# Kernel optimization log

Measured on AMD Instinct MI355X. Metric: run time of the kernel, lower is better.

Reference implementation:

```python
import jax, jax.numpy as jnp
import numpy as np

K = 5            # carafe kernel size
CK = 3           # content conv kernel size = max(3, K-2)
EMB = 64         # embedding size
FILTERS = 128    # output filters


def conv1x1(x, w, b=None):
    y = jnp.einsum('bhwc,co->bhwo', x, w)
    return y if b is None else y + b


def conv_same(x, w, b):
    y = jax.lax.conv_general_dilated(x, w, (1, 1), 'SAME',
                                     dimension_numbers=('NHWC', 'HWIO', 'NHWC'))
    return y + b


def up2(x):
    return jnp.repeat(jnp.repeat(x, 2, axis=1), 2, axis=2)


def setup_inputs() -> dict:
    key = jax.random.key(0)
    ks = jax.random.split(key, 12)
    B, H, W, Cf = 2, 128, 128, 128
    h, w, Cc = 64, 64, 128
    s = 0.05
    return {
        'fine': jax.random.normal(ks[0], (B, H, W, Cf), jnp.float32),
        'coarse': jax.random.normal(ks[1], (B, h, w, Cc), jnp.float32),
        # gate 1x1 conv (Cc -> 1)
        'w_gate': jax.random.normal(ks[2], (Cc, 1), jnp.float32) * s,
        'b_gate': jnp.zeros((1,), jnp.float32),
        # SemiShift: fine 1x1 (no bias), coarse 1x1 (bias), shared content conv (EMB -> K*K)
        'w_sfine': jax.random.normal(ks[3], (Cf, EMB), jnp.float32) * s,
        'w_scoarse': jax.random.normal(ks[4], (Cc, EMB), jnp.float32) * s,
        'b_scoarse': jnp.zeros((EMB,), jnp.float32),
        'w_content': jax.random.normal(ks[5], (CK, CK, EMB, K * K), jnp.float32) * s,
        'b_content': jnp.zeros((K * K,), jnp.float32),
        # output 1x1 convs
        'w_coarse': jax.random.normal(ks[6], (Cc, FILTERS), jnp.float32) * s,
        'b_coarse': jnp.zeros((FILTERS,), jnp.float32),
        'w_fineout': jax.random.normal(ks[7], (FILTERS, FILTERS), jnp.float32) * s,
        'b_fineout': jnp.zeros((FILTERS,), jnp.float32),
    }


def reference(fine, coarse, w_gate, b_gate, w_sfine, w_scoarse, b_scoarse,
              w_content, b_content, w_coarse, b_coarse, w_fineout, b_fineout):
    B, h, w, Cc = coarse.shape
    H, W = fine.shape[1], fine.shape[2]

    # gate branch
    gate = jax.nn.sigmoid(conv1x1(coarse, w_gate, b_gate))
    gate = up2(gate)  # [B,H,W,1]

    # SemiShift kernel prediction
    f = conv1x1(fine, w_sfine)                     # no bias
    f = conv_same(f, w_content, b_content)         # [B,H,W,K*K]
    c = conv1x1(coarse, w_scoarse, b_scoarse)
    c = conv_same(c, w_content, b_content)         # [B,h,w,K*K]
    kernel = jax.nn.softmax(f + up2(c), axis=-1)   # [B,H,W,K*K]

    # CarafeConvolution: extract_patches (TF layout: [pos, ch] innermost) + NN up + grouped matmul
    p = K // 2
    xp = jnp.pad(coarse, ((0, 0), (p, p), (p, p), (0, 0)))
    patches = jnp.stack([xp[:, r:r + h, cc:cc + w, :]
                         for r in range(K) for cc in range(K)], axis=3)  # [B,h,w,K*K,Cc]
    patches = patches.reshape(B, h, w, K * K * Cc)
    patches = up2(patches)                          # [B,H,W,K*K*Cc]
    # faithful reshape as in source (group_size=1): (B,H,W,Cc,K*K)
    feat = patches.reshape(B, H, W, Cc, K * K)
    carafe = jnp.einsum('bhwck,bhwk->bhwc', feat, kernel)  # [B,H,W,Cc]

    coarse_out = conv1x1(carafe, w_coarse, b_coarse)        # [B,H,W,FILTERS]
    fine_out = conv1x1(coarse_out, w_fineout, b_fineout)    # note: applied to coarse_out as in source
    return gate * fine_out + (1.0 - gate) * coarse_out
```

## Files before the change

kernel.cpp:

```cpp
#include <hip/hip_runtime.h>
#include <hip/hip_bf16.h>
#include <cstdint>
#include <cstddef>

#define KSZ 5
#define KK 25
#define EMB 64
#define CC 128
#define FILTERS 128

typedef __attribute__((ext_vector_type(8))) short short8;
typedef __attribute__((ext_vector_type(4))) float floatx4;

__device__ inline unsigned short f32_to_bf16(float f) {
    union { float f; unsigned u; } v; v.f = f;
    unsigned u = v.u;
    unsigned r = u + 0x7FFF + ((u >> 16) & 1);
    return (unsigned short)(r >> 16);
}

#define XS_P 136
__global__ __launch_bounds__(256) void embed_both_kernel(
        const float* __restrict__ xf, const float* __restrict__ wsf,
        const float* __restrict__ xc, const float* __restrict__ wsc,
        const float* __restrict__ bias_c,
        unsigned short* __restrict__ yf, unsigned short* __restrict__ yc,
        int nf, int nemb,
        const float* __restrict__ w_content, const float* __restrict__ w_coarse,
        const float* __restrict__ w_fineout,
        unsigned short* __restrict__ wconT, unsigned short* __restrict__ wcT,
        unsigned short* __restrict__ wfT) {
    int tid = threadIdx.x;

    if ((int)blockIdx.x >= nemb) {
        int idx = (blockIdx.x - nemb) * 256 + tid;
        if (idx < 18432) {
            int n = idx / 576, k = idx - n * 576;
            float v = (n < 25) ? w_content[k * 25 + n] : 0.0f;
            wconT[idx] = f32_to_bf16(v);
        } else if (idx < 34816) {
            int j = idx - 18432;
            int o = j >> 7, k = j & 127;
            wcT[j] = f32_to_bf16(w_coarse[k * 128 + o]);
        } else {
            int j = idx - 34816;
            int o = j >> 7, k = j & 127;
            wfT[j] = f32_to_bf16(w_fineout[k * 128 + o]);
        }
        return;
    }

    __shared__ unsigned short Xs[128 * XS_P];
    __shared__ unsigned short Ws[64 * XS_P];
    bool is_f = (int)blockIdx.x < nf;
    int blk = is_f ? blockIdx.x : (blockIdx.x - nf);
    const float* x = is_f ? xf : xc;
    const float* wsrcf = is_f ? wsf : wsc;
    const float* bias = is_f ? nullptr : bias_c;
    unsigned short* y = is_f ? yf : yc;
    size_t row0 = (size_t)blk * 128;

    {
        const float4* src = (const float4*)(x + row0 * 128);
        for (int ci = tid; ci < 4096; ci += 256) {
            int r = ci >> 5, c4 = ci & 31;
            float4 v = src[ci];
            uint2 u;
            u.x = (unsigned)f32_to_bf16(v.x) | ((unsigned)f32_to_bf16(v.y) << 16);
            u.y = (unsigned)f32_to_bf16(v.z) | ((unsigned)f32_to_bf16(v.w) << 16);
            *(uint2*)(&Xs[r * XS_P + c4 * 4]) = u;
        }
        for (int ci = tid; ci < 2048; ci += 256) {
            int k = ci >> 4;
            int n4 = (ci & 15) * 4;
            float4 v = *(const float4*)(wsrcf + k * 64 + n4);
            Ws[(n4 + 0) * XS_P + k] = f32_to_bf16(v.x);
            Ws[(n4 + 1) * XS_P + k] = f32_to_bf16(v.y);
            Ws[(n4 + 2) * XS_P + k] = f32_to_bf16(v.z);
            Ws[(n4 + 3) * XS_P + k] = f32_to_bf16(v.w);
        }
    }
    __syncthreads();

    int wid = tid >> 6, lane = tid & 63;
    int lr = lane & 15, hi = lane >> 4, lk = hi * 8;

    floatx4 acc[2][4];
    #pragma unroll
    for (int mi = 0; mi < 2; ++mi)
        #pragma unroll
        for (int ni = 0; ni < 4; ++ni)
            acc[mi][ni] = (floatx4){0.f, 0.f, 0.f, 0.f};

    #pragma unroll
    for (int kk = 0; kk < 128; kk += 32) {
        short8 a[2], bb[4];
        #pragma unroll
        for (int mi = 0; mi < 2; ++mi)
            a[mi] = *(const short8*)(&Xs[(wid * 32 + mi * 16 + lr) * XS_P + kk + lk]);
        #pragma unroll
        for (int ni = 0; ni < 4; ++ni)
            bb[ni] = *(const short8*)(&Ws[(ni * 16 + lr) * XS_P + kk + lk]);
        #pragma unroll
        for (int mi = 0; mi < 2; ++mi)
            #pragma unroll
            for (int ni = 0; ni < 4; ++ni)
                acc[mi][ni] = __builtin_amdgcn_mfma_f32_16x16x32_bf16(a[mi], bb[ni], acc[mi][ni], 0, 0, 0);
    }

    #pragma unroll
    for (int mi = 0; mi < 2; ++mi) {
        #pragma unroll
        for (int ni = 0; ni < 4; ++ni) {
            int col = ni * 16 + lr;
            float bs = bias ? bias[col] : 0.0f;
            #pragma unroll
            for (int j = 0; j < 4; ++j) {
                int row = wid * 32 + mi * 16 + hi * 4 + j;
                y[(row0 + row) * EMB + col] = f32_to_bf16(acc[mi][ni][j] + bs);
            }
        }
    }
}

#define SP 72
#define SB 584
__global__ __launch_bounds__(256) void content_both_kernel(
        const unsigned short* __restrict__ embf,
        const unsigned short* __restrict__ embc,
        const unsigned short* __restrict__ wT,
        const float* __restrict__ bias,
        float* __restrict__ yf, float* __restrict__ yc,
        int nf) {
    __shared__ unsigned short Es[6 * 34 * SP];
    __shared__ unsigned short Bs[32 * SB];
    int tid = threadIdx.x;
    bool is_f = (int)blockIdx.x < nf;
    int blk = is_f ? blockIdx.x : (blockIdx.x - nf);
    const unsigned short* emb = is_f ? embf : embc;
    float* y = is_f ? yf : yc;
    int HT = is_f ? 32 : 16;
    int WT = is_f ? 4 : 2;
    int Hh = is_f ? 128 : 64;
    int Ww = is_f ? 128 : 64;

    int bx = blk % WT;
    int t = blk / WT;
    int by = t % HT;
    int b = t / HT;

    for (int ci = tid; ci < 1632; ci += 256) {
        int pi = ci >> 3, e8 = ci & 7;
        int hy = pi / 34, hx = pi - hy * 34;
        int gy = by * 4 + hy - 1, gx = bx * 32 + hx - 1;
        uint4 v = {0u, 0u, 0u, 0u};
        if (gy >= 0 && gy < Hh && gx >= 0 && gx < Ww)
            v = *(const uint4*)(emb + (((size_t)(b * Hh + gy)) * Ww + gx) * EMB + e8 * 8);
        *(uint4*)(&Es[pi * SP + e8 * 8]) = v;
    }
    for (int ci = tid; ci < 2304; ci += 256) {
        int n = ci / 72, k8 = ci - n * 72;
        *(uint4*)(&Bs[n * SB + k8 * 8]) = *(const uint4*)(wT + n * 576 + k8 * 8);
    }
    __syncthreads();

    int wid = tid >> 6, lane = tid & 63;
    int lr = lane & 15, hi = lane >> 4, lk = hi * 8;

    floatx4 acc[2][2];
    #pragma unroll
    for (int mi = 0; mi < 2; ++mi)
        #pragma unroll
        for (int ni = 0; ni < 2; ++ni)
            acc[mi][ni] = (floatx4){0.f, 0.f, 0.f, 0.f};

    #pragma unroll
    for (int tap = 0; tap < 9; ++tap) {
        int dy = tap / 3, dx = tap - dy * 3;
        #pragma unroll
        for (int ks = 0; ks < 2; ++ks) {
            short8 a[2], bb[2];
            #pragma unroll
            for (int mi = 0; mi < 2; ++mi) {
                int p = wid * 32 + mi * 16 + lr;
                int r = p >> 5, c = p & 31;
                a[mi] = *(const short8*)(&Es[((r + dy) * 34 + (c + dx)) * SP + ks * 32 + lk]);
            }
            #pragma unroll
            for (int ni = 0; ni < 2; ++ni)
                bb[ni] = *(const short8*)(&Bs[(ni * 16 + lr) * SB + tap * 64 + ks * 32 + lk]);
            #pragma unroll
            for (int mi = 0; mi < 2; ++mi)
                #pragma unroll
                for (int ni = 0; ni < 2; ++ni)
                    acc[mi][ni] = __builtin_amdgcn_mfma_f32_16x16x32_bf16(a[mi], bb[ni], acc[mi][ni], 0, 0, 0);
        }
    }

    #pragma unroll
    for (int mi = 0; mi < 2; ++mi) {
        #pragma unroll
        for (int ni = 0; ni < 2; ++ni) {
            int n = ni * 16 + lr;
            if (n < KK) {
                float bs = bias[n];
                #pragma unroll
                for (int j = 0; j < 4; ++j) {
                    int p = wid * 32 + mi * 16 + hi * 4 + j;
                    int r = p >> 5, c = p & 31;
                    size_t gq = ((size_t)(b * Hh + by * 4 + r)) * Ww + bx * 32 + c;
                    y[gq * KK + n] = acc[mi][ni][j] + bs;
                }
            }
        }
    }
}

__global__ __launch_bounds__(256) void carafe_gate_kernel(
        const float* __restrict__ coarse,
        const float* __restrict__ f_conv,
        const float* __restrict__ c_conv,
        const float* __restrict__ w_gate,
        const float* __restrict__ b_gate,
        unsigned short* __restrict__ xout,
        float* __restrict__ g_gate,
        int h, int w) {
    __shared__ float patch[KK * CC];
    __shared__ float wsm[4 * 32];
    int cpix = blockIdx.x;
    int npix = h * w;
    int b = cpix / npix;
    int rem = cpix - b * npix;
    int cy = rem / w;
    int cx = rem - cy * w;
    int tid = threadIdx.x;

    for (int ci = tid; ci < 800; ci += 256) {
        int k = ci >> 5;
        int c4 = (ci & 31) << 2;
        int dy = (k * 205) >> 10;
        int dx = k - dy * 5;
        int py = cy + dy - 2, px = cx + dx - 2;
        float4 v = {0.f, 0.f, 0.f, 0.f};
        if (py >= 0 && py < h && px >= 0 && px < w)
            v = *(const float4*)(coarse + (((size_t)(b * h + py)) * w + px) * CC + c4);
        *(float4*)(&patch[ci << 2]) = v;
    }

    int wid = tid >> 6, lane = tid & 63;
    int H2 = 2 * h, W2 = 2 * w;
    {
        int fy = 2 * cy + (wid >> 1);
        int fx = 2 * cx + (wid & 1);
        size_t fq = ((size_t)(b * H2 + fy)) * W2 + fx;
        int k = lane & 31;
        float v = -1e30f;
        if (k < KK)
            v = f_conv[fq * KK + k] + c_conv[(size_t)cpix * KK + k];
        float m = v;
        #pragma unroll
        for (int mask = 16; mask > 0; mask >>= 1)
            m = fmaxf(m, __shfl_xor(m, mask, 32));
        float e = (k < KK) ? __expf(v - m) : 0.0f;
        float s = e;
        #pragma unroll
        for (int mask = 16; mask > 0; mask >>= 1)
            s += __shfl_xor(s, mask, 32);
        if (lane < 32)
            wsm[wid * 32 + k] = e / s;
    }
    __syncthreads();

    if (wid == 0) {
        float acc = patch[12 * CC + lane] * w_gate[lane]
                  + patch[12 * CC + lane + 64] * w_gate[lane + 64];
        #pragma unroll
        for (int off = 32; off > 0; off >>= 1)
            acc += __shfl_down(acc, off, 64);
        if (lane == 0) {
            float z = acc + b_gate[0];
            g_gate[cpix] = 1.0f / (1.0f + __expf(-z));
        }
    }

    {
        int ph = tid >> 7;
        int c = tid & 127;
        float w0[28], w1[28];
        #pragma unroll
        for (int j4 = 0; j4 < 7; ++j4) {
            *(float4*)(&w0[j4 * 4]) = *(const float4*)(&wsm[(2 * ph) * 32 + j4 * 4]);
            *(float4*)(&w1[j4 * 4]) = *(const float4*)(&wsm[(2 * ph + 1) * 32 + j4 * 4]);
        }
        const float* pp = patch + c * KK;
        float acc0 = 0.0f, acc1 = 0.0f;
        #pragma unroll
        for (int j = 0; j < KK; ++j) {
            float pv = pp[j];
            acc0 += w0[j] * pv;
            acc1 += w1[j] * pv;
        }
        int fy = 2 * cy + ph;
        size_t fq0 = ((size_t)(b * H2 + fy)) * W2 + 2 * cx;
        xout[fq0 * CC + c] = f32_to_bf16(acc0);
        xout[(fq0 + 1) * CC + c] = f32_to_bf16(acc1);
    }
}

#define LDSP 136
__global__ __launch_bounds__(256) void final_kernel(
        const unsigned short* __restrict__ X,
        const unsigned short* __restrict__ WcT,
        const unsigned short* __restrict__ WfT,
        const float* __restrict__ b_coarse,
        const float* __restrict__ b_fineout,
        const float* __restrict__ gate,
        float* __restrict__ out) {
    __shared__ unsigned short Xs[64 * LDSP];
    __shared__ unsigned short Ws[128 * LDSP];
    int tid = threadIdx.x;
    int row0 = blockIdx.x * 64;

    {
        const uint4* src = (const uint4*)(X + (size_t)row0 * 128);
        for (int ci = tid; ci < 1024; ci += 256) {
            int r = ci >> 4, c = ci & 15;
            *(uint4*)(&Xs[r * LDSP + c * 8]) = src[ci];
        }
        const uint4* wsrc = (const uint4*)WcT;
        for (int ci = tid; ci < 2048; ci += 256) {
            int r = ci >> 4, c = ci & 15;
            *(uint4*)(&Ws[r * LDSP + c * 8]) = wsrc[ci];
        }
    }
    __syncthreads();

    int wid = tid >> 6, lane = tid & 63;
    int wm = wid >> 1, wn = wid & 1;
    int lr = lane & 15;
    int lk = (lane >> 4) * 8;
    int lrow4 = (lane >> 4) * 4;

    floatx4 acc1[2][4];
    #pragma unroll
    for (int mi = 0; mi < 2; ++mi)
        #pragma unroll
        for (int ni = 0; ni < 4; ++ni)
            acc1[mi][ni] = (floatx4){0.f, 0.f, 0.f, 0.f};

    #pragma unroll
    for (int kk = 0; kk < 128; kk += 32) {
        short8 a[2], bb[4];
        #pragma unroll
        for (int mi = 0; mi < 2; ++mi)
            a[mi] = *(const short8*)(&Xs[(wm * 32 + mi * 16 + lr) * LDSP + kk + lk]);
        #pragma unroll
        for (int ni = 0; ni < 4; ++ni)
            bb[ni] = *(const short8*)(&Ws[(wn * 64 + ni * 16 + lr) * LDSP + kk + lk]);
        #pragma unroll
        for (int mi = 0; mi < 2; ++mi)
            #pragma unroll
            for (int ni = 0; ni < 4; ++ni)
                acc1[mi][ni] = __builtin_amdgcn_mfma_f32_16x16x32_bf16(a[mi], bb[ni], acc1[mi][ni], 0, 0, 0);
    }
    __syncthreads();

    {
        const uint4* wsrc = (const uint4*)WfT;
        for (int ci = tid; ci < 2048; ci += 256) {
            int r = ci >> 4, c = ci & 15;
            *(uint4*)(&Ws[r * LDSP + c * 8]) = wsrc[ci];
        }
    }
    #pragma unroll
    for (int mi = 0; mi < 2; ++mi) {
        #pragma unroll
        for (int ni = 0; ni < 4; ++ni) {
            int col = wn * 64 + ni * 16 + lr;
            float bc = b_coarse[col];
            #pragma unroll
            for (int j = 0; j < 4; ++j) {
                int row = wm * 32 + mi * 16 + lrow4 + j;
                float v = acc1[mi][ni][j] + bc;
                acc1[mi][ni][j] = v;
                Xs[row * LDSP + col] = f32_to_bf16(v);
            }
        }
    }
    __syncthreads();

    floatx4 acc2[2][4];
    #pragma unroll
    for (int mi = 0; mi < 2; ++mi)
        #pragma unroll
        for (int ni = 0; ni < 4; ++ni)
            acc2[mi][ni] = (floatx4){0.f, 0.f, 0.f, 0.f};

    #pragma unroll
    for (int kk = 0; kk < 128; kk += 32) {
        short8 a[2], bb[4];
        #pragma unroll
        for (int mi = 0; mi < 2; ++mi)
            a[mi] = *(const short8*)(&Xs[(wm * 32 + mi * 16 + lr) * LDSP + kk + lk]);
        #pragma unroll
        for (int ni = 0; ni < 4; ++ni)
            bb[ni] = *(const short8*)(&Ws[(wn * 64 + ni * 16 + lr) * LDSP + kk + lk]);
        #pragma unroll
        for (int mi = 0; mi < 2; ++mi)
            #pragma unroll
            for (int ni = 0; ni < 4; ++ni)
                acc2[mi][ni] = __builtin_amdgcn_mfma_f32_16x16x32_bf16(a[mi], bb[ni], acc2[mi][ni], 0, 0, 0);
    }

    #pragma unroll
    for (int mi = 0; mi < 2; ++mi) {
        #pragma unroll
        for (int ni = 0; ni < 4; ++ni) {
            int col = wn * 64 + ni * 16 + lr;
            float bf = b_fineout[col];
            #pragma unroll
            for (int j = 0; j < 4; ++j) {
                int row = wm * 32 + mi * 16 + lrow4 + j;
                int q = row0 + row;
                int b = q >> 14;
                int remq = q & 16383;
                int fy = remq >> 7, fx = remq & 127;
                float g = gate[(b << 12) + ((fy >> 1) << 6) + (fx >> 1)];
                float co = acc1[mi][ni][j];
                float fo = acc2[mi][ni][j] + bf;
                out[(size_t)q * FILTERS + col] = g * fo + (1.0f - g) * co;
            }
        }
    }
}

extern "C" void kernel_launch(void* const* d_in, const int* in_sizes, int n_in,
                              void* d_out, int out_size, void* d_ws, size_t ws_size,
                              hipStream_t stream) {
    const float* fine      = (const float*)d_in[0];
    const float* coarse    = (const float*)d_in[1];
    const float* w_gate    = (const float*)d_in[2];
    const float* b_gate    = (const float*)d_in[3];
    const float* w_sfine   = (const float*)d_in[4];
    const float* w_scoarse = (const float*)d_in[5];
    const float* b_scoarse = (const float*)d_in[6];
    const float* w_content = (const float*)d_in[7];
    const float* b_content = (const float*)d_in[8];
    const float* w_coarse  = (const float*)d_in[9];
    const float* b_coarse  = (const float*)d_in[10];
    const float* w_fineout = (const float*)d_in[11];
    const float* b_fineout = (const float*)d_in[12];
    float* out = (float*)d_out;

    const int B = 2, H = 128, W = 128, h = 64, w = 64;
    const int MF = B * H * W;
    const int MC = B * h * w;

    char* ws = (char*)d_ws;
    size_t off = 0;
    auto alloc = [&](size_t bytes) {
        void* p = ws + off;
        off = (off + bytes + 255) & ~(size_t)255;
        return p;
    };
    float* g_gate            = (float*)alloc((size_t)MC * 4);
    unsigned short* f_emb    = (unsigned short*)alloc((size_t)MF * EMB * 2);
    unsigned short* c_emb    = (unsigned short*)alloc((size_t)MC * EMB * 2);
    float* f_conv            = (float*)alloc((size_t)MF * KK * 4);
    float* c_conv            = (float*)alloc((size_t)MC * KK * 4);
    unsigned short* x_bf16   = (unsigned short*)alloc((size_t)MF * CC * 2);
    unsigned short* wconT    = (unsigned short*)alloc(32 * 576 * 2);
    unsigned short* wcT      = (unsigned short*)alloc(128 * 128 * 2);
    unsigned short* wfT      = (unsigned short*)alloc(128 * 128 * 2);

    const int NEF = MF / 128;
    const int NEC = MC / 128;
    const int NEB = NEF + NEC;
    const int NWT = 200;
    const int NCF = B * (H / 4) * (W / 32);
    const int NCC = B * (h / 4) * (w / 32);

    embed_both_kernel<<<NEB + NWT, 256, 0, stream>>>(fine, w_sfine, coarse, w_scoarse, b_scoarse,
                                                     f_emb, c_emb, NEF, NEB,
                                                     w_content, w_coarse, w_fineout,
                                                     wconT, wcT, wfT);
    content_both_kernel<<<NCF + NCC, 256, 0, stream>>>(f_emb, c_emb, wconT, b_content,
                                                       f_conv, c_conv, NCF);
    carafe_gate_kernel<<<MC, 256, 0, stream>>>(coarse, f_conv, c_conv, w_gate, b_gate,
                                               x_bf16, g_gate, h, w);
    final_kernel<<<MF / 64, 256, 0, stream>>>(x_bf16, wcT, wfT, b_coarse, b_fineout, g_gate, out);
}
```

Baseline: 54.05 us.

## Fuse CARAFE reassembly and gate into final MFMA GEMM kernel with tiled patches

Merges the carafe/gate kernel and the final two-GEMM kernel into one. Each block handles a 4x4 coarse tile (8x8 fine pixels = 64 rows). It loads an 8x8 coarse halo once into LDS and reuses it across 16 coarse pixels. The bf16 carafe result and the gate values stay in shared memory, so the global round trip of x_bf16 and g_gate and one launch are removed. The cost is fewer blocks (512) with large LDS (~58KB) and serial per-thread loops, which lowers occupancy.

```diff
diff --git a/kernel.cpp b/kernel.cpp
--- a/kernel.cpp
+++ b/kernel.cpp
@@ -216,117 +216,129 @@
     }
 }
 
-__global__ __launch_bounds__(256) void carafe_gate_kernel(
+#define LDSP 136
+__global__ __launch_bounds__(256) void carafe_final_kernel(
         const float* __restrict__ coarse,
         const float* __restrict__ f_conv,
         const float* __restrict__ c_conv,
         const float* __restrict__ w_gate,
         const float* __restrict__ b_gate,
-        unsigned short* __restrict__ xout,
-        float* __restrict__ g_gate,
-        int h, int w) {
-    __shared__ float patch[KK * CC];
-    __shared__ float wsm[4 * 32];
-    int cpix = blockIdx.x;
-    int npix = h * w;
-    int b = cpix / npix;
-    int rem = cpix - b * npix;
-    int cy = rem / w;
-    int cx = rem - cy * w;
-    int tid = threadIdx.x;
-
-    for (int ci = tid; ci < 800; ci += 256) {
-        int k = ci >> 5;
-        int c4 = (ci & 31) << 2;
-        int dy = (k * 205) >> 10;
-        int dx = k - dy * 5;
-        int py = cy + dy - 2, px = cx + dx - 2;
-        float4 v = {0.f, 0.f, 0.f, 0.f};
-        if (py >= 0 && py < h && px >= 0 && px < w)
-            v = *(const float4*)(coarse + (((size_t)(b * h + py)) * w + px) * CC + c4);
-        *(float4*)(&patch[ci << 2]) = v;
-    }
-
-    int wid = tid >> 6, lane = tid & 63;
-    int H2 = 2 * h, W2 = 2 * w;
-    {
-        int fy = 2 * cy + (wid >> 1);
-        int fx = 2 * cx + (wid & 1);
-        size_t fq = ((size_t)(b * H2 + fy)) * W2 + fx;
-        int k = lane & 31;
-        float v = -1e30f;
-        if (k < KK)
-            v = f_conv[fq * KK + k] + c_conv[(size_t)cpix * KK + k];
-        float m = v;
-        #pragma unroll
-        for (int mask = 16; mask > 0; mask >>= 1)
-            m = fmaxf(m, __shfl_xor(m, mask, 32));
-        float e = (k < KK) ? __expf(v - m) : 0.0f;
-        float s = e;
-        #pragma unroll
-        for (int mask = 16; mask > 0; mask >>= 1)
-            s += __shfl_xor(s, mask, 32);
-        if (lane < 32)
-            wsm[wid * 32 + k] = e / s;
-    }
-    __syncthreads();
-
-    if (wid == 0) {
-        float acc = patch[12 * CC + lane] * w_gate[lane]
-                  + patch[12 * CC + lane + 64] * w_gate[lane + 64];
-        #pragma unroll
-        for (int off = 32; off > 0; off >>= 1)
-            acc += __shfl_down(acc, off, 64);
-        if (lane == 0) {
-            float z = acc + b_gate[0];
-            g_gate[cpix] = 1.0f / (1.0f + __expf(-z));
-        }
-    }
-
-    {
-        int ph = tid >> 7;
-        int c = tid & 127;
-        float w0[28], w1[28];
-        #pragma unroll
-        for (int j4 = 0; j4 < 7; ++j4) {
-            *(float4*)(&w0[j4 * 4]) = *(const float4*)(&wsm[(2 * ph) * 32 + j4 * 4]);
-            *(float4*)(&w1[j4 * 4]) = *(const float4*)(&wsm[(2 * ph + 1) * 32 + j4 * 4]);
-        }
-        const float* pp = patch + c * KK;
-        float acc0 = 0.0f, acc1 = 0.0f;
-        #pragma unroll
-        for (int j = 0; j < KK; ++j) {
-            float pv = pp[j];
-            acc0 += w0[j] * pv;
-            acc1 += w1[j] * pv;
-        }
-        int fy = 2 * cy + ph;
-        size_t fq0 = ((size_t)(b * H2 + fy)) * W2 + 2 * cx;
-        xout[fq0 * CC + c] = f32_to_bf16(acc0);
-        xout[(fq0 + 1) * CC + c] = f32_to_bf16(acc1);
-    }
-}
-
-#define LDSP 136
-__global__ __launch_bounds__(256) void final_kernel(
-        const unsigned short* __restrict__ X,
         const unsigned short* __restrict__ WcT,
         const unsigned short* __restrict__ WfT,
         const float* __restrict__ b_coarse,
         const float* __restrict__ b_fineout,
-        const float* __restrict__ gate,
         float* __restrict__ out) {
-    __shared__ unsigned short Xs[64 * LDSP];
-    __shared__ unsigned short Ws[128 * LDSP];
+    __shared__ __align__(16) char smem[58624];
+    float* patches = (float*)smem;
+    float* wsm     = (float*)(smem + 32768);
+    float* g_lds   = (float*)(smem + 40960);
+    unsigned short* Ws = (unsigned short*)smem;
+    unsigned short* Xs = (unsigned short*)(smem + 41216);
+
+    const int h = 64, w = 64, H2 = 128, W2 = 128;
     int tid = threadIdx.x;
-    int row0 = blockIdx.x * 64;
-
-    {
-        const uint4* src = (const uint4*)(X + (size_t)row0 * 128);
-        for (int ci = tid; ci < 1024; ci += 256) {
-            int r = ci >> 4, c = ci & 15;
-            *(uint4*)(&Xs[r * LDSP + c * 8]) = src[ci];
-        }
+    int blk = blockIdx.x;
+    int cx0 = (blk & 15) * 4;
+    int cy0 = ((blk >> 4) & 15) * 4;
+    int b = blk >> 8;
+
+    for (int ci = tid; ci < 2048; ci += 256) {
+        int pi = ci >> 5;
+        int c4 = (ci & 31) << 2;
+        int sy = cy0 - 2 + (pi >> 3);
+        int sx = cx0 - 2 + (pi & 7);
+        float4 v = {0.f, 0.f, 0.f, 0.f};
+        if (sy >= 0 && sy < h && sx >= 0 && sx < w)
+            v = *(const float4*)(coarse + (((size_t)(b * h + sy)) * w + sx) * CC + c4);
+        *(float4*)(&patches[pi * 128 + c4]) = v;
+    }
+
+    int wid = tid >> 6, lane = tid & 63;
+    {
+        int k = lane & 31;
+        #pragma unroll
+        for (int pass = 0; pass < 8; ++pass) {
+            int fp = wid * 16 + pass * 2 + (lane >> 5);
+            int fry = fp >> 3, frx = fp & 7;
+            int fy = 2 * cy0 + fry, fx = 2 * cx0 + frx;
+            int cy = cy0 + (fry >> 1), cx = cx0 + (frx >> 1);
+            size_t fq = ((size_t)(b * H2 + fy)) * W2 + fx;
+            size_t cq = ((size_t)(b * h + cy)) * w + cx;
+            float v = -1e30f;
+            if (k < KK)
+                v = f_conv[fq * KK + k] + c_conv[cq * KK + k];
+            float m = v;
+            #pragma unroll
+            for (int mask = 16; mask > 0; mask >>= 1)
+                m = fmaxf(m, __shfl_xor(m, mask, 32));
+            float e = (k < KK) ? __expf(v - m) : 0.0f;
+            float s = e;
+            #pragma unroll
+            for (int mask = 16; mask > 0; mask >>= 1)
+                s += __shfl_xor(s, mask, 32);
+            wsm[fp * 32 + k] = e / s;
+        }
+    }
+    __syncthreads();
+
+    {
+        int cp = tid >> 4;
+        int part = tid & 15;
+        int pidx = ((cp >> 2) + 2) * 8 + (cp & 3) + 2;
+        const float* pc = patches + pidx * 128 + part * 8;
+        float4 a0 = *(const float4*)(pc);
+        float4 a1 = *(const float4*)(pc + 4);
+        float4 g0 = *(const float4*)(w_gate + part * 8);
+        float4 g1 = *(const float4*)(w_gate + part * 8 + 4);
+        float acc = a0.x * g0.x + a0.y * g0.y + a0.z * g0.z + a0.w * g0.w
+                  + a1.x * g1.x + a1.y * g1.y + a1.z * g1.z + a1.w * g1.w;
+        #pragma unroll
+        for (int mask = 8; mask > 0; mask >>= 1)
+            acc += __shfl_xor(acc, mask, 16);
+        if (part == 0) {
+            float z = acc + b_gate[0];
+            g_lds[cp] = 1.0f / (1.0f + __expf(-z));
+        }
+    }
+
+    {
+        int ph = tid >> 7;
+        int c  = tid & 127;
+        int offs[KK];
+        int c25 = c * 25;
+        #pragma unroll
+        for (int j = 0; j < KK; ++j) {
+            int i = c25 + j;
+            int p = i >> 7;
+            int ch = i & 127;
+            int pd = (p * 205) >> 10;
+            int pm = p - pd * 5;
+            offs[j] = (pd * 8 + pm) * 128 + ch;
+        }
+        for (int cp = 0; cp < 16; ++cp) {
+            int ry = cp >> 2, rx = cp & 3;
+            int cpbase = (ry * 8 + rx) * 128;
+            int fpA = (2 * ry + ph) * 8 + 2 * rx;
+            float w0[28], w1[28];
+            #pragma unroll
+            for (int j4 = 0; j4 < 7; ++j4) {
+                *(float4*)(&w0[j4 * 4]) = *(const float4*)(&wsm[fpA * 32 + j4 * 4]);
+                *(float4*)(&w1[j4 * 4]) = *(const float4*)(&wsm[(fpA + 1) * 32 + j4 * 4]);
+            }
+            float acc0 = 0.0f, acc1 = 0.0f;
+            #pragma unroll
+            for (int j = 0; j < KK; ++j) {
+                float pv = patches[cpbase + offs[j]];
+                acc0 += w0[j] * pv;
+                acc1 += w1[j] * pv;
+            }
+            Xs[fpA * LDSP + c] = f32_to_bf16(acc0);
+            Xs[(fpA + 1) * LDSP + c] = f32_to_bf16(acc1);
+        }
+    }
+    __syncthreads();
+
+    {
         const uint4* wsrc = (const uint4*)WcT;
         for (int ci = tid; ci < 2048; ci += 256) {
             int r = ci >> 4, c = ci & 15;
@@ -335,7 +347,6 @@
     }
     __syncthreads();
 
-    int wid = tid >> 6, lane = tid & 63;
     int wm = wid >> 1, wn = wid & 1;
     int lr = lane & 15;
     int lk = (lane >> 4) * 8;
@@ -421,14 +432,13 @@
             #pragma unroll
             for (int j = 0; j < 4; ++j) {
                 int row = wm * 32 + mi * 16 + lrow4 + j;
-                int q = row0 + row;
-                int b = q >> 14;
-                int remq = q & 16383;
-                int fy = remq >> 7, fx = remq & 127;
-                float g = gate[(b << 12) + ((fy >> 1) << 6) + (fx >> 1)];
+                int fry = row >> 3, frx = row & 7;
+                float g = g_lds[((fry >> 1) << 2) + (frx >> 1)];
+                int fy = 2 * cy0 + fry, fx = 2 * cx0 + frx;
+                size_t q = ((size_t)(b * H2 + fy)) * W2 + fx;
                 float co = acc1[mi][ni][j];
                 float fo = acc2[mi][ni][j] + bf;
-                out[(size_t)q * FILTERS + col] = g * fo + (1.0f - g) * co;
+                out[q * FILTERS + col] = g * fo + (1.0f - g) * co;
             }
         }
     }
@@ -463,12 +473,10 @@
         off = (off + bytes + 255) & ~(size_t)255;
         return p;
     };
-    float* g_gate            = (float*)alloc((size_t)MC * 4);
     unsigned short* f_emb    = (unsigned short*)alloc((size_t)MF * EMB * 2);
     unsigned short* c_emb    = (unsigned short*)alloc((size_t)MC * EMB * 2);
     float* f_conv            = (float*)alloc((size_t)MF * KK * 4);
     float* c_conv            = (float*)alloc((size_t)MC * KK * 4);
-    unsigned short* x_bf16   = (unsigned short*)alloc((size_t)MF * CC * 2);
     unsigned short* wconT    = (unsigned short*)alloc(32 * 576 * 2);
     unsigned short* wcT      = (unsigned short*)alloc(128 * 128 * 2);
     unsigned short* wfT      = (unsigned short*)alloc(128 * 128 * 2);
@@ -486,7 +494,6 @@
                                                      wconT, wcT, wfT);
     content_both_kernel<<<NCF + NCC, 256, 0, stream>>>(f_emb, c_emb, wconT, b_content,
                                                        f_conv, c_conv, NCF);
-    carafe_gate_kernel<<<MC, 256, 0, stream>>>(coarse, f_conv, c_conv, w_gate, b_gate,
-                                               x_bf16, g_gate, h, w);
-    final_kernel<<<MF / 64, 256, 0, stream>>>(x_bf16, wcT, wfT, b_coarse, b_fineout, g_gate, out);
+    carafe_final_kernel<<<B * 16 * 16, 256, 0, stream>>>(coarse, f_conv, c_conv, w_gate, b_gate,
+                                                         wcT, wfT, b_coarse, b_fineout, out);
 }
```

After: 49.96 us, median of 2. 7.6% less time.
